# Performance work log

Hardware: AMD Instinct MI355X
Metric: run time of the kernel (lower is better)

## Reference

```python
import jax, jax.numpy as jnp
import numpy as np

B, S, DQK, DV, H = 4, 2048, 128, 128, 8


def setup_inputs() -> dict:
    key = jax.random.key(0)
    ks = jax.random.split(key, 9)
    s = 0.02
    return {
        "query": jax.random.normal(ks[0], (B, S, DQK), jnp.float32),
        "key": jax.random.normal(ks[1], (B, S, DQK), jnp.float32),
        "value": jax.random.normal(ks[2], (B, S, DV), jnp.float32),
        "WQ": jax.random.normal(ks[3], (DQK, H * DQK), jnp.float32) * s,
        "bQ": jax.random.normal(ks[4], (H * DQK,), jnp.float32) * s,
        "WK": jax.random.normal(ks[5], (DQK, H * DQK), jnp.float32) * s,
        "bK": jax.random.normal(ks[6], (H * DQK,), jnp.float32) * s,
        "WV": jax.random.normal(ks[7], (DV, H * DV), jnp.float32) * s,
        "bV": jax.random.normal(ks[8], (H * DV,), jnp.float32) * s,
    }


def reference(query, key, value, WQ, bQ, WK, bK, WV, bV):
    b, qn, dqk = query.shape
    kn = key.shape[1]
    dv = value.shape[2]
    h = H
    # projections -> [b, n, h, d]
    Q = (query @ WQ + bQ).reshape(b, qn, h, dqk)
    K = (key @ WK + bK).reshape(b, kn, h, dqk)
    V = (value @ WV + bV).reshape(b, kn, h, dv)
    # abs(QK^T)/sqrt(dk) score -- non-standard, prevents flash kernels
    scores = jnp.abs(jnp.einsum("bqhd,bkhd->bhqk", Q, K)) / jnp.sqrt(
        jnp.asarray(dqk, query.dtype)
    )
    w = jax.nn.softmax(scores, axis=-1)  # [b,h,q,k]
    # (complex cast +0j in the original is numerically a no-op on real V)
    out = jnp.einsum("bhqk,bkhd->bqhd", w, V).reshape(b, qn, h * dv)
    return out
```

## Files before the change

### kernel.cpp

```cpp
#include <hip/hip_runtime.h>
#include <hip/hip_bf16.h>

#define B_ 4
#define S_ 2048
#define D_ 128
#define H_ 8

typedef __attribute__((ext_vector_type(8))) short bf16x8;
typedef __attribute__((ext_vector_type(4))) float f32x4;

__device__ __forceinline__ short f2bf(float f) {
  union { float f; unsigned u; } v; v.f = f;
  unsigned u = v.u;
  unsigned r = (u + 0x7FFFu + ((u >> 16) & 1u)) >> 16;
  return (short)r;
}

__device__ __forceinline__ short4 pack4(f32x4 p) {
  union { __hip_bfloat162 h2[2]; short4 s4; } u;
  u.h2[0] = __float22bfloat162_rn(make_float2(p[0], p[1]));
  u.h2[1] = __float22bfloat162_rn(make_float2(p[2], p[3]));
  return u.s4;
}

__device__ __forceinline__ void dma16(const short* g, short* l) {
  __builtin_amdgcn_global_load_lds(
      (const __attribute__((address_space(1))) unsigned int*)g,
      (__attribute__((address_space(3))) unsigned int*)l, 16, 0, 0);
}

__global__ void cvt3(const float* __restrict__ a, const float* __restrict__ b,
                     const float* __restrict__ c, short* __restrict__ oa,
                     short* __restrict__ ob, short* __restrict__ oc) {
  int i = blockIdx.x * 256 + threadIdx.x;
  int which = i >> 18;
  int j = i & 262143;
  const float* in = (which == 0) ? a : (which == 1) ? b : c;
  short* out = (which == 0) ? oa : (which == 1) ? ob : oc;
  float4 v = ((const float4*)in)[j];
  short4 o = make_short4(f2bf(v.x), f2bf(v.y), f2bf(v.z), f2bf(v.w));
  ((short4*)out)[j] = o;
}

__global__ __launch_bounds__(256) void transpose3(const float* __restrict__ WQ, const float* __restrict__ WK,
                                                  const float* __restrict__ WV, short* __restrict__ TQ,
                                                  short* __restrict__ TK, short* __restrict__ TV) {
  __shared__ float tile[64][65];
  int bw = blockIdx.x >> 5;
  int tl = blockIdx.x & 31;
  int n0 = (tl & 15) * 64, k0 = (tl >> 4) * 64;
  const float* W = (bw == 0) ? WQ : (bw == 1) ? WK : WV;
  short* Wt = (bw == 0) ? TQ : (bw == 1) ? TK : TV;
#pragma unroll
  for (int i = 0; i < 16; ++i) {
    int c = threadIdx.x + 256 * i;
    int rr = c >> 6, cc = c & 63;
    tile[rr][cc] = W[(k0 + rr) * 1024 + n0 + cc];
  }
  __syncthreads();
#pragma unroll
  for (int i = 0; i < 16; ++i) {
    int c = threadIdx.x + 256 * i;
    int rr = c >> 6, cc = c & 63;
    Wt[(n0 + rr) * 128 + k0 + cc] = f2bf(tile[cc][rr]);
  }
}

template <int WA>
__device__ __forceinline__ void proj_tile(const short* __restrict__ X,
                                          const short* __restrict__ Wt,
                                          const float* __restrict__ bias,
                                          short* __restrict__ out,
                                          int mtile, int ntile,
                                          short* sA, short* sB) {
  int tid = threadIdx.x;
  int lane = tid & 63, w = tid >> 6;
  int l15 = lane & 15, l4 = lane >> 4;
  int m0 = mtile * 128, n0 = ntile * 128;

#pragma unroll
  for (int j = 0; j < 8; ++j) {
    int f = w * 8 + j;
    const short* src = X + (m0 + (f >> 2) * 16 + l15) * 128 + (f & 3) * 32 + l4 * 8;
    dma16(src, sA + f * 512);
  }
#pragma unroll
  for (int j = 0; j < 8; ++j) {
    int f = w * 8 + j;
    const short* src = Wt + (n0 + (f >> 2) * 16 + l15) * 128 + (f & 3) * 32 + l4 * 8;
    dma16(src, sB + f * 512);
  }
  __syncthreads();

  int wr = w >> 1, wc = w & 1;
  f32x4 acc[4][4];
#pragma unroll
  for (int mi = 0; mi < 4; ++mi)
#pragma unroll
    for (int ni = 0; ni < 4; ++ni) acc[mi][ni] = (f32x4){0.f, 0.f, 0.f, 0.f};

#pragma unroll
  for (int mi = 0; mi < 4; ++mi) {
    bf16x8 a[4];
#pragma unroll
    for (int st = 0; st < 4; ++st)
      a[st] = *(const bf16x8*)(sA + ((wr * 4 + mi) * 4 + st) * 512 + lane * 8);
#pragma unroll
    for (int ni = 0; ni < 4; ++ni) {
#pragma unroll
      for (int st = 0; st < 4; ++st) {
        bf16x8 b = *(const bf16x8*)(sB + ((wc * 4 + ni) * 4 + st) * 512 + lane * 8);
        if (WA)
          acc[mi][ni] = __builtin_amdgcn_mfma_f32_16x16x32_bf16(b, a[st], acc[mi][ni], 0, 0, 0);
        else
          acc[mi][ni] = __builtin_amdgcn_mfma_f32_16x16x32_bf16(a[st], b, acc[mi][ni], 0, 0, 0);
      }
    }
  }

  if (WA) {
#pragma unroll
    for (int mi = 0; mi < 4; ++mi) {
      int sg = m0 + wr * 64 + mi * 16 + l15;
      int bb = sg >> 11, s = sg & 2047;
      short* orow = out + ((size_t)(bb * H_ + ntile) * S_ + s) * D_;
#pragma unroll
      for (int ni = 0; ni < 4; ++ni) {
        int d0 = wc * 64 + ni * 16 + l4 * 4;
        float4 bv = *(const float4*)(bias + n0 + d0);
        f32x4 t = acc[mi][ni];
        t[0] += bv.x; t[1] += bv.y; t[2] += bv.z; t[3] += bv.w;
        *(short4*)(orow + d0) = pack4(t);
      }
    }
  } else {
#pragma unroll
    for (int ni = 0; ni < 4; ++ni) {
      int d = wc * 64 + ni * 16 + l15;
      float bv = bias[n0 + d];
#pragma unroll
      for (int mi = 0; mi < 4; ++mi) {
        int sg0 = m0 + wr * 64 + mi * 16 + l4 * 4;
        int bb = sg0 >> 11, s0 = sg0 & 2047;
        f32x4 t = acc[mi][ni];
        t[0] += bv; t[1] += bv; t[2] += bv; t[3] += bv;
        *(short4*)(out + ((size_t)(bb * H_ + ntile) * D_ + d) * S_ + s0) = pack4(t);
      }
    }
  }
}

__global__ __launch_bounds__(256, 2) void proj3(
    const short* __restrict__ xq, const short* __restrict__ xk, const short* __restrict__ xv,
    const short* __restrict__ wtq, const short* __restrict__ wtk, const short* __restrict__ wtv,
    const float* __restrict__ bQ, const float* __restrict__ bK, const float* __restrict__ bV,
    short* __restrict__ Qp, short* __restrict__ Kp, short* __restrict__ Vt) {
  __shared__ short sA[16384], sB[16384];
  int work = (blockIdx.x & 7) * 192 + (blockIdx.x >> 3);
  int which = work >> 9;
  int t = work & 511;
  int mtile = t >> 3, ntile = t & 7;
  if (which == 0)      proj_tile<1>(xq, wtq, bQ, Qp, mtile, ntile, sA, sB);
  else if (which == 1) proj_tile<1>(xk, wtk, bK, Kp, mtile, ntile, sA, sB);
  else                 proj_tile<0>(xv, wtv, bV, Vt, mtile, ntile, sA, sB);
}

#define BN 64
#define PSTR 72

#define ATTN_ITER(KB, VB, KN, VN, IT)                                          \
  {                                                                            \
    if ((IT) + 1 < S_ / BN) {                                                  \
      int kt_ = ((IT) + 1) * BN;                                               \
      const short* kgs = kg + kt_ * D_;                                        \
      short* kl = (KN) + (w * 4) * 512;                                        \
      dma16(kgs, kl);                                                          \
      dma16(kgs + 32, kl + 512);                                               \
      dma16(kgs + 64, kl + 1024);                                              \
      dma16(kgs + 96, kl + 1536);                                              \
      short* vl = (VN) + (w * 4) * 512;                                        \
      dma16(vg0 + kt_, vl);                                                    \
      dma16(vg0 + kt_ + 32, vl + 512);                                         \
      dma16(vg1 + kt_, vl + 1024);                                             \
      dma16(vg1 + kt_ + 32, vl + 1536);                                        \
    }                                                                          \
             \
    f32x4 s0[4], s1[4];                                                        \
    _Pragma("unroll") for (int mt = 0; mt < 4; ++mt) {                         \
      s0[mt] = (f32x4){0.f, 0.f, 0.f, 0.f};                                    \
      s1[mt] = (f32x4){0.f, 0.f, 0.f, 0.f};                                    \
      _Pragma("unroll") for (int st = 0; st < 4; ++st) {                       \
        bf16x8 bk = *(const bf16x8*)((KB) + (mt * 4 + st) * 512 + lane * 8);   \
        s0[mt] = __builtin_amdgcn_mfma_f32_16x16x32_bf16(bk, aq[0][st], s0[mt], 0, 0, 0); \
        s1[mt] = __builtin_amdgcn_mfma_f32_16x16x32_bf16(bk, aq[1][st], s1[mt], 0, 0, 0); \
      }                                                                        \
    }                                                                          \
     \
    bf16x8 ap0[2], ap1[2];                                                     \
    _Pragma("unroll") for (int mt = 0; mt < 4; ++mt) {                         \
      _Pragma("unroll") for (int r = 0; r < 4; ++r) {                          \
        float p = __builtin_amdgcn_exp2f(fabsf(s0[mt][r]) * SC2);              \
        ls0 += p;                                                              \
        s0[mt][r] = p;                                                         \
      }                                                                        \
      *(short4*)(pw + l15 * PSTR + mt * 16 + l4 * 4) = pack4(s0[mt]);          \
    }                                                                          \
    ap0[0] = *(const bf16x8*)(pw + l15 * PSTR + l4 * 8);                       \
    ap0[1] = *(const bf16x8*)(pw + l15 * PSTR + 32 + l4 * 8);                  \
      \
    _Pragma("unroll") for (int mt = 0; mt < 4; ++mt) {                         \
      _Pragma("unroll") for (int r = 0; r < 4; ++r) {                          \
        float p = __builtin_amdgcn_exp2f(fabsf(s1[mt][r]) * SC2);              \
        ls1 += p;                                                              \
        s1[mt][r] = p;                                                         \
      }                                                                        \
      *(short4*)(pw + l15 * PSTR + mt * 16 + l4 * 4) = pack4(s1[mt]);          \
    }                                                                          \
    ap1[0] = *(const bf16x8*)(pw + l15 * PSTR + l4 * 8);                       \
    ap1[1] = *(const bf16x8*)(pw + l15 * PSTR + 32 + l4 * 8);                  \
                       \
    _Pragma("unroll") for (int t = 0; t < 8; ++t) {                            \
      _Pragma("unroll") for (int kst = 0; kst < 2; ++kst) {                    \
        bf16x8 bv = *(const bf16x8*)((VB) + (t * 2 + kst) * 512 + lane * 8);   \
        o0[t] = __builtin_amdgcn_mfma_f32_16x16x32_bf16(ap0[kst], bv, o0[t], 0, 0, 0); \
        o1[t] = __builtin_amdgcn_mfma_f32_16x16x32_bf16(ap1[kst], bv, o1[t], 0, 0, 0); \
      }                                                                        \
    }                                                                          \
    __syncthreads();   \
  }

__global__ __launch_bounds__(256, 2) void attn(const short* __restrict__ Qp,
                                               const short* __restrict__ Kp,
                                               const short* __restrict__ Vt,
                                               float* __restrict__ out) {
  __shared__ short sK0[8192], sK1[8192];
  __shared__ short sV0[8192], sV1[8192];
  __shared__ short sP[4 * 16 * PSTR];

  int tid = threadIdx.x;
  int lane = tid & 63, w = tid >> 6;
  int qt = blockIdx.x & 15;
  int bh = blockIdx.x >> 4;
  int q0 = qt * 128;
  int l15 = lane & 15, l4 = lane >> 4;

  const short* Qbase = Qp + (size_t)bh * S_ * D_;
  const short* Kbase = Kp + (size_t)bh * S_ * D_;
  const short* Vbase = Vt + (size_t)bh * D_ * S_;

  const short* kg = Kbase + (w * 16 + l15) * D_ + l4 * 8;
  const short* vg0 = Vbase + ((2 * w) * 16 + l15) * S_ + l4 * 8;
  const short* vg1 = Vbase + ((2 * w + 1) * 16 + l15) * S_ + l4 * 8;

  {
    short* kl = sK0 + (w * 4) * 512;
    dma16(kg, kl);
    dma16(kg + 32, kl + 512);
    dma16(kg + 64, kl + 1024);
    dma16(kg + 96, kl + 1536);
    short* vl = sV0 + (w * 4) * 512;
    dma16(vg0, vl);
    dma16(vg0 + 32, vl + 512);
    dma16(vg1, vl + 1024);
    dma16(vg1 + 32, vl + 1536);
  }

  bf16x8 aq[2][4];
#pragma unroll
  for (int g = 0; g < 2; ++g)
#pragma unroll
    for (int st = 0; st < 4; ++st)
      aq[g][st] = *(const bf16x8*)(Qbase + (q0 + w * 32 + g * 16 + l15) * D_ + l4 * 8 + 32 * st);

  f32x4 o0[8], o1[8];
#pragma unroll
  for (int t = 0; t < 8; ++t) {
    o0[t] = (f32x4){0.f, 0.f, 0.f, 0.f};
    o1[t] = (f32x4){0.f, 0.f, 0.f, 0.f};
  }
  float ls0 = 0.f, ls1 = 0.f;

  const float SC2 = 0.127530637f;
  short* pw = sP + w * 16 * PSTR;

  __syncthreads();

  for (int it = 0; it < S_ / BN; it += 2) {
    ATTN_ITER(sK0, sV0, sK1, sV1, it);
    ATTN_ITER(sK1, sV1, sK0, sV0, it + 1);
  }

  ls0 += __shfl_xor(ls0, 16);
  ls0 += __shfl_xor(ls0, 32);
  ls1 += __shfl_xor(ls1, 16);
  ls1 += __shfl_xor(ls1, 32);
  float inv0[4], inv1[4];
#pragma unroll
  for (int r = 0; r < 4; ++r) {
    inv0[r] = 1.f / __shfl(ls0, l4 * 4 + r);
    inv1[r] = 1.f / __shfl(ls1, l4 * 4 + r);
  }

  int bb = bh >> 3, h = bh & 7;
#pragma unroll
  for (int t = 0; t < 8; ++t) {
#pragma unroll
    for (int r = 0; r < 4; ++r) {
      int qA = q0 + w * 32 + l4 * 4 + r;
      int qB = qA + 16;
      out[((size_t)(bb * S_ + qA)) * (H_ * D_) + h * D_ + t * 16 + l15] = o0[t][r] * inv0[r];
      out[((size_t)(bb * S_ + qB)) * (H_ * D_) + h * D_ + t * 16 + l15] = o1[t][r] * inv1[r];
    }
  }
}

extern "C" void kernel_launch(void* const* d_in, const int* in_sizes, int n_in,
                              void* d_out, int out_size, void* d_ws, size_t ws_size,
                              hipStream_t stream) {
  (void)in_sizes; (void)n_in; (void)out_size; (void)ws_size;
  const float* q  = (const float*)d_in[0];
  const float* k  = (const float*)d_in[1];
  const float* v  = (const float*)d_in[2];
  const float* WQ = (const float*)d_in[3];
  const float* bQ = (const float*)d_in[4];
  const float* WK = (const float*)d_in[5];
  const float* bK = (const float*)d_in[6];
  const float* WV = (const float*)d_in[7];
  const float* bV = (const float*)d_in[8];

  const int NX = B_ * S_ * D_;
  const int NW = D_ * H_ * D_;
  const int NP = B_ * H_ * S_ * D_;

  short* ws  = (short*)d_ws;
  short* xq  = ws;
  short* xk  = xq + NX;
  short* xv  = xk + NX;
  short* wtq = xv + NX;
  short* wtk = wtq + NW;
  short* wtv = wtk + NW;
  short* Qp  = wtv + NW;
  short* Kp  = Qp + NP;
  short* Vt  = Kp + NP;

  cvt3<<<3 * (NX / 4) / 256, 256, 0, stream>>>(q, k, v, xq, xk, xv);
  transpose3<<<96, 256, 0, stream>>>(WQ, WK, WV, wtq, wtk, wtv);

  proj3<<<1536, 256, 0, stream>>>(xq, xk, xv, wtq, wtk, wtv, bQ, bK, bV, Qp, Kp, Vt);

  attn<<<512, 256, 0, stream>>>(Qp, Kp, Vt, (float*)d_out);
}
```

Measured before the change: 193.3 us.

## Load V tiles directly into registers, merge prep kernels, add priority hints and swizzle

The attention kernel no longer stages V through double-buffered LDS. Each wave now loads its V fragments straight from global memory into registers, split into two halves around the QK^T MFMA block, which frees half of the kernel's LDS. s_setprio is raised around the MFMA sections, and the block index is swizzled to change which (batch, head, q-tile) runs where. The separate input-convert and weight-transpose kernels are fused into one launch to save a kernel launch. The trade-off is that all four waves now fetch the same V data from global memory, which relies on L1/L2 hits and may expose load latency.

```diff
diff --git a/kernel.cpp b/kernel.cpp
--- a/kernel.cpp
+++ b/kernel.cpp
@@ -29,40 +29,41 @@
       (__attribute__((address_space(3))) unsigned int*)l, 16, 0, 0);
 }
 
-__global__ void cvt3(const float* __restrict__ a, const float* __restrict__ b,
-                     const float* __restrict__ c, short* __restrict__ oa,
-                     short* __restrict__ ob, short* __restrict__ oc) {
-  int i = blockIdx.x * 256 + threadIdx.x;
-  int which = i >> 18;
-  int j = i & 262143;
-  const float* in = (which == 0) ? a : (which == 1) ? b : c;
-  short* out = (which == 0) ? oa : (which == 1) ? ob : oc;
-  float4 v = ((const float4*)in)[j];
-  short4 o = make_short4(f2bf(v.x), f2bf(v.y), f2bf(v.z), f2bf(v.w));
-  ((short4*)out)[j] = o;
-}
-
-__global__ __launch_bounds__(256) void transpose3(const float* __restrict__ WQ, const float* __restrict__ WK,
-                                                  const float* __restrict__ WV, short* __restrict__ TQ,
-                                                  short* __restrict__ TK, short* __restrict__ TV) {
+__global__ __launch_bounds__(256) void prep(
+    const float* __restrict__ a, const float* __restrict__ b, const float* __restrict__ c,
+    short* __restrict__ oa, short* __restrict__ ob, short* __restrict__ oc,
+    const float* __restrict__ WQ, const float* __restrict__ WK, const float* __restrict__ WV,
+    short* __restrict__ TQ, short* __restrict__ TK, short* __restrict__ TV) {
   __shared__ float tile[64][65];
-  int bw = blockIdx.x >> 5;
-  int tl = blockIdx.x & 31;
-  int n0 = (tl & 15) * 64, k0 = (tl >> 4) * 64;
-  const float* W = (bw == 0) ? WQ : (bw == 1) ? WK : WV;
-  short* Wt = (bw == 0) ? TQ : (bw == 1) ? TK : TV;
-#pragma unroll
-  for (int i = 0; i < 16; ++i) {
-    int c = threadIdx.x + 256 * i;
-    int rr = c >> 6, cc = c & 63;
-    tile[rr][cc] = W[(k0 + rr) * 1024 + n0 + cc];
-  }
-  __syncthreads();
-#pragma unroll
-  for (int i = 0; i < 16; ++i) {
-    int c = threadIdx.x + 256 * i;
-    int rr = c >> 6, cc = c & 63;
-    Wt[(n0 + rr) * 128 + k0 + cc] = f2bf(tile[cc][rr]);
+  if (blockIdx.x < 3072) {
+    int i = blockIdx.x * 256 + threadIdx.x;
+    int which = i >> 18;
+    int j = i & 262143;
+    const float* in = (which == 0) ? a : (which == 1) ? b : c;
+    short* out = (which == 0) ? oa : (which == 1) ? ob : oc;
+    float4 v = ((const float4*)in)[j];
+    short4 o = make_short4(f2bf(v.x), f2bf(v.y), f2bf(v.z), f2bf(v.w));
+    ((short4*)out)[j] = o;
+  } else {
+    int bid = blockIdx.x - 3072;
+    int bw = bid >> 5;
+    int tl = bid & 31;
+    int n0 = (tl & 15) * 64, k0 = (tl >> 4) * 64;
+    const float* W = (bw == 0) ? WQ : (bw == 1) ? WK : WV;
+    short* Wt = (bw == 0) ? TQ : (bw == 1) ? TK : TV;
+#pragma unroll
+    for (int i = 0; i < 16; ++i) {
+      int cix = threadIdx.x + 256 * i;
+      int rr = cix >> 6, cc = cix & 63;
+      tile[rr][cc] = W[(k0 + rr) * 1024 + n0 + cc];
+    }
+    __syncthreads();
+#pragma unroll
+    for (int i = 0; i < 16; ++i) {
+      int cix = threadIdx.x + 256 * i;
+      int rr = cix >> 6, cc = cix & 63;
+      Wt[(n0 + rr) * 128 + k0 + cc] = f2bf(tile[cc][rr]);
+    }
   }
 }
 
@@ -168,8 +169,9 @@
 #define BN 64
 #define PSTR 72
 
-#define ATTN_ITER(KB, VB, KN, VN, IT)                                          \
+#define ATTN_ITER(KB, KN, IT)                                                  \
   {                                                                            \
+    const int kb_ = (IT) * BN;                                                 \
     if ((IT) + 1 < S_ / BN) {                                                  \
       int kt_ = ((IT) + 1) * BN;                                               \
       const short* kgs = kg + kt_ * D_;                                        \
@@ -178,14 +180,16 @@
       dma16(kgs + 32, kl + 512);                                               \
       dma16(kgs + 64, kl + 1024);                                              \
       dma16(kgs + 96, kl + 1536);                                              \
-      short* vl = (VN) + (w * 4) * 512;                                        \
-      dma16(vg0 + kt_, vl);                                                    \
-      dma16(vg0 + kt_ + 32, vl + 512);                                         \
-      dma16(vg1 + kt_, vl + 1024);                                             \
-      dma16(vg1 + kt_ + 32, vl + 1536);                                        \
+    }                                                                          \
+             \
+    bf16x8 bv[16];                                                             \
+    _Pragma("unroll") for (int tt = 0; tt < 4; ++tt) {                         \
+      bv[tt * 2]     = *(const bf16x8*)(vp + tt * 16 * S_ + kb_);              \
+      bv[tt * 2 + 1] = *(const bf16x8*)(vp + tt * 16 * S_ + kb_ + 32);         \
     }                                                                          \
              \
     f32x4 s0[4], s1[4];                                                        \
+    __builtin_amdgcn_s_setprio(1);                                             \
     _Pragma("unroll") for (int mt = 0; mt < 4; ++mt) {                         \
       s0[mt] = (f32x4){0.f, 0.f, 0.f, 0.f};                                    \
       s1[mt] = (f32x4){0.f, 0.f, 0.f, 0.f};                                    \
@@ -194,6 +198,12 @@
         s0[mt] = __builtin_amdgcn_mfma_f32_16x16x32_bf16(bk, aq[0][st], s0[mt], 0, 0, 0); \
         s1[mt] = __builtin_amdgcn_mfma_f32_16x16x32_bf16(bk, aq[1][st], s1[mt], 0, 0, 0); \
       }                                                                        \
+    }                                                                          \
+    __builtin_amdgcn_s_setprio(0);                                             \
+                        \
+    _Pragma("unroll") for (int tt = 4; tt < 8; ++tt) {                         \
+      bv[tt * 2]     = *(const bf16x8*)(vp + tt * 16 * S_ + kb_);              \
+      bv[tt * 2 + 1] = *(const bf16x8*)(vp + tt * 16 * S_ + kb_ + 32);         \
     }                                                                          \
      \
     bf16x8 ap0[2], ap1[2];                                                     \
@@ -207,7 +217,7 @@
     }                                                                          \
     ap0[0] = *(const bf16x8*)(pw + l15 * PSTR + l4 * 8);                       \
     ap0[1] = *(const bf16x8*)(pw + l15 * PSTR + 32 + l4 * 8);                  \
-      \
+                 \
     _Pragma("unroll") for (int mt = 0; mt < 4; ++mt) {                         \
       _Pragma("unroll") for (int r = 0; r < 4; ++r) {                          \
         float p = __builtin_amdgcn_exp2f(fabsf(s1[mt][r]) * SC2);              \
@@ -218,15 +228,16 @@
     }                                                                          \
     ap1[0] = *(const bf16x8*)(pw + l15 * PSTR + l4 * 8);                       \
     ap1[1] = *(const bf16x8*)(pw + l15 * PSTR + 32 + l4 * 8);                  \
-                       \
+                      \
+    __builtin_amdgcn_s_setprio(1);                                             \
     _Pragma("unroll") for (int t = 0; t < 8; ++t) {                            \
       _Pragma("unroll") for (int kst = 0; kst < 2; ++kst) {                    \
-        bf16x8 bv = *(const bf16x8*)((VB) + (t * 2 + kst) * 512 + lane * 8);   \
-        o0[t] = __builtin_amdgcn_mfma_f32_16x16x32_bf16(ap0[kst], bv, o0[t], 0, 0, 0); \
-        o1[t] = __builtin_amdgcn_mfma_f32_16x16x32_bf16(ap1[kst], bv, o1[t], 0, 0, 0); \
+        o0[t] = __builtin_amdgcn_mfma_f32_16x16x32_bf16(ap0[kst], bv[t * 2 + kst], o0[t], 0, 0, 0); \
+        o1[t] = __builtin_amdgcn_mfma_f32_16x16x32_bf16(ap1[kst], bv[t * 2 + kst], o1[t], 0, 0, 0); \
       }                                                                        \
     }                                                                          \
-    __syncthreads();   \
+    __builtin_amdgcn_s_setprio(0);                                             \
+    __syncthreads();     \
   }
 
 __global__ __launch_bounds__(256, 2) void attn(const short* __restrict__ Qp,
@@ -234,13 +245,13 @@
                                                const short* __restrict__ Vt,
                                                float* __restrict__ out) {
   __shared__ short sK0[8192], sK1[8192];
-  __shared__ short sV0[8192], sV1[8192];
   __shared__ short sP[4 * 16 * PSTR];
 
   int tid = threadIdx.x;
   int lane = tid & 63, w = tid >> 6;
-  int qt = blockIdx.x & 15;
-  int bh = blockIdx.x >> 4;
+  int swz = (blockIdx.x & 7) * 64 + (blockIdx.x >> 3);
+  int qt = swz & 15;
+  int bh = swz >> 4;
   int q0 = qt * 128;
   int l15 = lane & 15, l4 = lane >> 4;
 
@@ -249,8 +260,7 @@
   const short* Vbase = Vt + (size_t)bh * D_ * S_;
 
   const short* kg = Kbase + (w * 16 + l15) * D_ + l4 * 8;
-  const short* vg0 = Vbase + ((2 * w) * 16 + l15) * S_ + l4 * 8;
-  const short* vg1 = Vbase + ((2 * w + 1) * 16 + l15) * S_ + l4 * 8;
+  const short* vp = Vbase + l15 * S_ + l4 * 8;
 
   {
     short* kl = sK0 + (w * 4) * 512;
@@ -258,11 +268,6 @@
     dma16(kg + 32, kl + 512);
     dma16(kg + 64, kl + 1024);
     dma16(kg + 96, kl + 1536);
-    short* vl = sV0 + (w * 4) * 512;
-    dma16(vg0, vl);
-    dma16(vg0 + 32, vl + 512);
-    dma16(vg1, vl + 1024);
-    dma16(vg1 + 32, vl + 1536);
   }
 
   bf16x8 aq[2][4];
@@ -286,8 +291,8 @@
   __syncthreads();
 
   for (int it = 0; it < S_ / BN; it += 2) {
-    ATTN_ITER(sK0, sV0, sK1, sV1, it);
-    ATTN_ITER(sK1, sV1, sK0, sV0, it + 1);
+    ATTN_ITER(sK0, sK1, it);
+    ATTN_ITER(sK1, sK0, it + 1);
   }
 
   ls0 += __shfl_xor(ls0, 16);
@@ -343,8 +348,7 @@
   short* Kp  = Qp + NP;
   short* Vt  = Kp + NP;
 
-  cvt3<<<3 * (NX / 4) / 256, 256, 0, stream>>>(q, k, v, xq, xk, xv);
-  transpose3<<<96, 256, 0, stream>>>(WQ, WK, WV, wtq, wtk, wtv);
+  prep<<<3168, 256, 0, stream>>>(q, k, v, xq, xk, xv, WQ, WK, WV, wtq, wtk, wtv);
 
   proj3<<<1536, 256, 0, stream>>>(xq, xk, xv, wtq, wtk, wtv, bQ, bK, bV, Qp, Kp, Vt);
 
```

After: 264.7 us. +36.9%, slower.
